# Optimization experiments

Measured on AMD Instinct MI355X. Metric: run time of the kernel, lower is better.

The kernel has to match this reference:

```python
import jax, jax.numpy as jnp
import numpy as np
from jax import lax

SYM = 128
STATES = 2
T = 4194304


def setup_inputs() -> dict:
    key = jax.random.key(0)
    k_tok, k_ls, k_fin = jax.random.split(key, 3)
    tokens = jax.random.randint(k_tok, (T,), 0, SYM, dtype=jnp.int64 if jax.config.jax_enable_x64 else jnp.int32)
    # original init: ones / states / states; add noise so grads are non-degenerate
    ls = jnp.ones((SYM, STATES, STATES), dtype=jnp.float32) / (STATES * STATES)
    ls = ls + 0.01 * jax.random.normal(k_ls, (SYM, STATES, STATES), dtype=jnp.float32)
    final = jnp.ones((STATES, 1), dtype=jnp.float32)
    return {"tokens": tokens, "ls": ls, "final": final}


def reference(tokens, ls, final):
    # initial state vector [1, 0] (hardcoded in the original forward)
    states = ls.shape[1]
    v0 = jnp.zeros((states,), dtype=ls.dtype).at[0].set(1.0)

    def step(v, j):
        # gather the 2x2 transition for symbol j and advance: v <- v @ ls[j]
        return v @ ls[j], None

    v, _ = lax.scan(step, v0, tokens)
    # faithful to the original: the last token's matrix is applied a second time
    v = v @ ls[tokens[-1]]
    return v
```

## Files before the change

kernel.cpp:

```cpp
#include <hip/hip_runtime.h>


#define T_TOKENS 4194304
#define TPB      512
#define TOKS     16
#define BLOCKS   (T_TOKENS / (TPB * TOKS))

typedef float v2f __attribute__((ext_vector_type(2)));

__device__ __forceinline__ float4 mm(const float4 A, const float4 B) {
    const v2f Br0 = {B.x, B.y};
    const v2f Br1 = {B.z, B.w};
    const v2f c0 = A.x * Br0 + A.y * Br1;
    const v2f c1 = A.z * Br0 + A.w * Br1;
    return make_float4(c0.x, c0.y, c1.x, c1.y);
}

template <int N>
__device__ __forceinline__ float4 dpp_shr4(const float4 m) {
    float4 o;
    o.x = __int_as_float(__builtin_amdgcn_update_dpp(
        __float_as_int(m.x), __float_as_int(m.x), 0x110 | N, 0xF, 0xF, false));
    o.y = __int_as_float(__builtin_amdgcn_update_dpp(
        __float_as_int(m.y), __float_as_int(m.y), 0x110 | N, 0xF, 0xF, false));
    o.z = __int_as_float(__builtin_amdgcn_update_dpp(
        __float_as_int(m.z), __float_as_int(m.z), 0x110 | N, 0xF, 0xF, false));
    o.w = __int_as_float(__builtin_amdgcn_update_dpp(
        __float_as_int(m.w), __float_as_int(m.w), 0x110 | N, 0xF, 0xF, false));
    return o;
}

template <int XMASK>
__device__ __forceinline__ float4 swz_xor4(const float4 m) {
    constexpr int OFF = (XMASK << 10) | 0x1F;
    float4 o;
    o.x = __int_as_float(__builtin_amdgcn_ds_swizzle(__float_as_int(m.x), OFF));
    o.y = __int_as_float(__builtin_amdgcn_ds_swizzle(__float_as_int(m.y), OFF));
    o.z = __int_as_float(__builtin_amdgcn_ds_swizzle(__float_as_int(m.z), OFF));
    o.w = __int_as_float(__builtin_amdgcn_ds_swizzle(__float_as_int(m.w), OFF));
    return o;
}

__device__ __forceinline__ float4 wave_reduce_mm(float4 m) {
    m = mm(m, dpp_shr4<1>(m));
    m = mm(m, dpp_shr4<2>(m));
    m = mm(m, dpp_shr4<4>(m));
    m = mm(m, dpp_shr4<8>(m));
    m = mm(m, swz_xor4<16>(m));
    m = mm(m, swz_xor4<32>(m));
    return m;
}

__global__ __launch_bounds__(TPB) void scan_phase1(const int4* __restrict__ tok4,
                                                   const float4* __restrict__ ls,
                                                   float4* __restrict__ partials) {
    __shared__ float4 s_ls[128];
    __shared__ float4 sm[8];

    const int tid = threadIdx.x;
    if (tid < 128) s_ls[tid] = ls[tid];
    __syncthreads();

    const int4* p = tok4 + (size_t)(blockIdx.x * TPB + tid) * (TOKS / 4);
    const int4 t0 = p[0];
    const int4 t1 = p[1];
    const int4 t2 = p[2];
    const int4 t3 = p[3];

    float4 m = s_ls[t0.x];
    m = mm(m, s_ls[t0.y]);
    m = mm(m, s_ls[t0.z]);
    m = mm(m, s_ls[t0.w]);
    m = mm(m, s_ls[t1.x]);
    m = mm(m, s_ls[t1.y]);
    m = mm(m, s_ls[t1.z]);
    m = mm(m, s_ls[t1.w]);
    m = mm(m, s_ls[t2.x]);
    m = mm(m, s_ls[t2.y]);
    m = mm(m, s_ls[t2.z]);
    m = mm(m, s_ls[t2.w]);
    m = mm(m, s_ls[t3.x]);
    m = mm(m, s_ls[t3.y]);
    m = mm(m, s_ls[t3.z]);
    m = mm(m, s_ls[t3.w]);

    m = wave_reduce_mm(m);

    if ((tid & 63) == 0) sm[tid >> 6] = m;
    __syncthreads();
    if (tid == 0) {
        const float4 q01 = mm(sm[0], sm[1]);
        const float4 q23 = mm(sm[2], sm[3]);
        const float4 q45 = mm(sm[4], sm[5]);
        const float4 q67 = mm(sm[6], sm[7]);
        partials[blockIdx.x] = mm(mm(q01, q23), mm(q45, q67));
    }
}

__global__ __launch_bounds__(TPB) void scan_phase2(const float4* __restrict__ partials,
                                                   const int* __restrict__ tokens,
                                                   const float4* __restrict__ ls,
                                                   float* __restrict__ out) {
    const int tid = threadIdx.x;
    float4 m = partials[tid];

    m = wave_reduce_mm(m);

    __shared__ float4 sf[8];
    if ((tid & 63) == 0) sf[tid >> 6] = m;
    __syncthreads();
    if (tid == 0) {
        const float4 q01 = mm(sf[0], sf[1]);
        const float4 q23 = mm(sf[2], sf[3]);
        const float4 q45 = mm(sf[4], sf[5]);
        const float4 q67 = mm(sf[6], sf[7]);
        float4 M = mm(mm(q01, q23), mm(q45, q67));
        M = mm(M, ls[tokens[T_TOKENS - 1]]);
        out[0] = M.x;
        out[1] = M.y;
    }
}

extern "C" void kernel_launch(void* const* d_in, const int* in_sizes, int n_in,
                              void* d_out, int out_size, void* d_ws, size_t ws_size,
                              hipStream_t stream) {
    const int*    tokens = (const int*)d_in[0];
    const float4* ls     = (const float4*)d_in[1];
    float*  out      = (float*)d_out;
    float4* partials = (float4*)d_ws;

    scan_phase1<<<BLOCKS, TPB, 0, stream>>>((const int4*)tokens, ls, partials);
    scan_phase2<<<1, TPB, 0, stream>>>(partials, tokens, ls, out);
}
```

Before: 66.95 us.

## Double tokens per thread, split LDS rows, and use row_bcast DPP wave reduction

Each thread now multiplies 32 tokens as two independent 16-token chains, which halves the block count and adds instruction-level parallelism. The LDS table is split into two row arrays of float2, and the wave reduction drops ds_swizzle in favour of DPP row_bcast15/31 with the result read from lane 63. Phase 2 shrinks to 256 threads to match the 256 partials. The approach relies on the operand order in the row_bcast reduction being correct for non-commutative matrix products, and longer per-thread work may reduce latency hiding.

```diff
diff --git a/kernel.cpp b/kernel.cpp
--- a/kernel.cpp
+++ b/kernel.cpp
@@ -3,121 +3,126 @@
 
 #define T_TOKENS 4194304
 #define TPB      512
-#define TOKS     16
+#define TOKS     32
 #define BLOCKS   (T_TOKENS / (TPB * TOKS))
+#define TPB2     256
 
 typedef float v2f __attribute__((ext_vector_type(2)));
 
-__device__ __forceinline__ float4 mm(const float4 A, const float4 B) {
-    const v2f Br0 = {B.x, B.y};
-    const v2f Br1 = {B.z, B.w};
-    const v2f c0 = A.x * Br0 + A.y * Br1;
-    const v2f c1 = A.z * Br0 + A.w * Br1;
-    return make_float4(c0.x, c0.y, c1.x, c1.y);
+struct m22 { v2f r0, r1; };
+
+__device__ __forceinline__ m22 mm(const m22 A, const m22 B) {
+    m22 C;
+    C.r0 = A.r0.x * B.r0 + A.r0.y * B.r1;
+    C.r1 = A.r1.x * B.r0 + A.r1.y * B.r1;
+    return C;
 }
 
-template <int N>
-__device__ __forceinline__ float4 dpp_shr4(const float4 m) {
-    float4 o;
-    o.x = __int_as_float(__builtin_amdgcn_update_dpp(
-        __float_as_int(m.x), __float_as_int(m.x), 0x110 | N, 0xF, 0xF, false));
-    o.y = __int_as_float(__builtin_amdgcn_update_dpp(
-        __float_as_int(m.y), __float_as_int(m.y), 0x110 | N, 0xF, 0xF, false));
-    o.z = __int_as_float(__builtin_amdgcn_update_dpp(
-        __float_as_int(m.z), __float_as_int(m.z), 0x110 | N, 0xF, 0xF, false));
-    o.w = __int_as_float(__builtin_amdgcn_update_dpp(
-        __float_as_int(m.w), __float_as_int(m.w), 0x110 | N, 0xF, 0xF, false));
+__device__ __forceinline__ float4 to4(const m22 m) {
+    return make_float4(m.r0.x, m.r0.y, m.r1.x, m.r1.y);
+}
+__device__ __forceinline__ m22 fr4(const float4 f) {
+    return m22{ (v2f){f.x, f.y}, (v2f){f.z, f.w} };
+}
+
+template <int CTRL, int ROWM>
+__device__ __forceinline__ m22 dpp4(const m22 m) {
+    m22 o;
+    o.r0.x = __int_as_float(__builtin_amdgcn_update_dpp(
+        __float_as_int(m.r0.x), __float_as_int(m.r0.x), CTRL, ROWM, 0xF, false));
+    o.r0.y = __int_as_float(__builtin_amdgcn_update_dpp(
+        __float_as_int(m.r0.y), __float_as_int(m.r0.y), CTRL, ROWM, 0xF, false));
+    o.r1.x = __int_as_float(__builtin_amdgcn_update_dpp(
+        __float_as_int(m.r1.x), __float_as_int(m.r1.x), CTRL, ROWM, 0xF, false));
+    o.r1.y = __int_as_float(__builtin_amdgcn_update_dpp(
+        __float_as_int(m.r1.y), __float_as_int(m.r1.y), CTRL, ROWM, 0xF, false));
     return o;
 }
 
-template <int XMASK>
-__device__ __forceinline__ float4 swz_xor4(const float4 m) {
-    constexpr int OFF = (XMASK << 10) | 0x1F;
-    float4 o;
-    o.x = __int_as_float(__builtin_amdgcn_ds_swizzle(__float_as_int(m.x), OFF));
-    o.y = __int_as_float(__builtin_amdgcn_ds_swizzle(__float_as_int(m.y), OFF));
-    o.z = __int_as_float(__builtin_amdgcn_ds_swizzle(__float_as_int(m.z), OFF));
-    o.w = __int_as_float(__builtin_amdgcn_ds_swizzle(__float_as_int(m.w), OFF));
-    return o;
-}
-
-__device__ __forceinline__ float4 wave_reduce_mm(float4 m) {
-    m = mm(m, dpp_shr4<1>(m));
-    m = mm(m, dpp_shr4<2>(m));
-    m = mm(m, dpp_shr4<4>(m));
-    m = mm(m, dpp_shr4<8>(m));
-    m = mm(m, swz_xor4<16>(m));
-    m = mm(m, swz_xor4<32>(m));
+__device__ __forceinline__ m22 wave_reduce_hi(m22 m) {
+    m = mm(dpp4<0x101, 0xF>(m), m);
+    m = mm(dpp4<0x102, 0xF>(m), m);
+    m = mm(dpp4<0x104, 0xF>(m), m);
+    m = mm(dpp4<0x108, 0xF>(m), m);
+    m = mm(dpp4<0x142, 0xA>(m), m);
+    m = mm(dpp4<0x143, 0xC>(m), m);
     return m;
 }
 
 __global__ __launch_bounds__(TPB) void scan_phase1(const int4* __restrict__ tok4,
                                                    const float4* __restrict__ ls,
                                                    float4* __restrict__ partials) {
-    __shared__ float4 s_ls[128];
+    __shared__ v2f s_r0[128];
+    __shared__ v2f s_r1[128];
     __shared__ float4 sm[8];
 
     const int tid = threadIdx.x;
-    if (tid < 128) s_ls[tid] = ls[tid];
+    if (tid < 128) {
+        const float4 e = ls[tid];
+        s_r0[tid] = (v2f){e.x, e.y};
+        s_r1[tid] = (v2f){e.z, e.w};
+    }
     __syncthreads();
+
+#define LDM(i) (m22{ s_r0[(i)], s_r1[(i)] })
 
     const int4* p = tok4 + (size_t)(blockIdx.x * TPB + tid) * (TOKS / 4);
     const int4 t0 = p[0];
     const int4 t1 = p[1];
     const int4 t2 = p[2];
     const int4 t3 = p[3];
+    const int4 t4 = p[4];
+    const int4 t5 = p[5];
+    const int4 t6 = p[6];
+    const int4 t7 = p[7];
 
-    float4 m = s_ls[t0.x];
-    m = mm(m, s_ls[t0.y]);
-    m = mm(m, s_ls[t0.z]);
-    m = mm(m, s_ls[t0.w]);
-    m = mm(m, s_ls[t1.x]);
-    m = mm(m, s_ls[t1.y]);
-    m = mm(m, s_ls[t1.z]);
-    m = mm(m, s_ls[t1.w]);
-    m = mm(m, s_ls[t2.x]);
-    m = mm(m, s_ls[t2.y]);
-    m = mm(m, s_ls[t2.z]);
-    m = mm(m, s_ls[t2.w]);
-    m = mm(m, s_ls[t3.x]);
-    m = mm(m, s_ls[t3.y]);
-    m = mm(m, s_ls[t3.z]);
-    m = mm(m, s_ls[t3.w]);
+    m22 a = LDM(t0.x);
+    a = mm(a, LDM(t0.y)); a = mm(a, LDM(t0.z)); a = mm(a, LDM(t0.w));
+    a = mm(a, LDM(t1.x)); a = mm(a, LDM(t1.y)); a = mm(a, LDM(t1.z)); a = mm(a, LDM(t1.w));
+    a = mm(a, LDM(t2.x)); a = mm(a, LDM(t2.y)); a = mm(a, LDM(t2.z)); a = mm(a, LDM(t2.w));
+    a = mm(a, LDM(t3.x)); a = mm(a, LDM(t3.y)); a = mm(a, LDM(t3.z)); a = mm(a, LDM(t3.w));
 
-    m = wave_reduce_mm(m);
+    m22 b = LDM(t4.x);
+    b = mm(b, LDM(t4.y)); b = mm(b, LDM(t4.z)); b = mm(b, LDM(t4.w));
+    b = mm(b, LDM(t5.x)); b = mm(b, LDM(t5.y)); b = mm(b, LDM(t5.z)); b = mm(b, LDM(t5.w));
+    b = mm(b, LDM(t6.x)); b = mm(b, LDM(t6.y)); b = mm(b, LDM(t6.z)); b = mm(b, LDM(t6.w));
+    b = mm(b, LDM(t7.x)); b = mm(b, LDM(t7.y)); b = mm(b, LDM(t7.z)); b = mm(b, LDM(t7.w));
 
-    if ((tid & 63) == 0) sm[tid >> 6] = m;
+    m22 m = mm(a, b);
+
+    m = wave_reduce_hi(m);
+
+    if ((tid & 63) == 63) sm[tid >> 6] = to4(m);
     __syncthreads();
     if (tid == 0) {
-        const float4 q01 = mm(sm[0], sm[1]);
-        const float4 q23 = mm(sm[2], sm[3]);
-        const float4 q45 = mm(sm[4], sm[5]);
-        const float4 q67 = mm(sm[6], sm[7]);
-        partials[blockIdx.x] = mm(mm(q01, q23), mm(q45, q67));
+        const m22 q01 = mm(fr4(sm[0]), fr4(sm[1]));
+        const m22 q23 = mm(fr4(sm[2]), fr4(sm[3]));
+        const m22 q45 = mm(fr4(sm[4]), fr4(sm[5]));
+        const m22 q67 = mm(fr4(sm[6]), fr4(sm[7]));
+        partials[blockIdx.x] = to4(mm(mm(q01, q23), mm(q45, q67)));
     }
+#undef LDM
 }
 
-__global__ __launch_bounds__(TPB) void scan_phase2(const float4* __restrict__ partials,
-                                                   const int* __restrict__ tokens,
-                                                   const float4* __restrict__ ls,
-                                                   float* __restrict__ out) {
+__global__ __launch_bounds__(TPB2) void scan_phase2(const float4* __restrict__ partials,
+                                                    const int* __restrict__ tokens,
+                                                    const float4* __restrict__ ls,
+                                                    float* __restrict__ out) {
     const int tid = threadIdx.x;
-    float4 m = partials[tid];
+    m22 m = fr4(partials[tid]);
 
-    m = wave_reduce_mm(m);
+    m = wave_reduce_hi(m);
 
-    __shared__ float4 sf[8];
-    if ((tid & 63) == 0) sf[tid >> 6] = m;
+    __shared__ float4 sf[4];
+    if ((tid & 63) == 63) sf[tid >> 6] = to4(m);
     __syncthreads();
     if (tid == 0) {
-        const float4 q01 = mm(sf[0], sf[1]);
-        const float4 q23 = mm(sf[2], sf[3]);
-        const float4 q45 = mm(sf[4], sf[5]);
-        const float4 q67 = mm(sf[6], sf[7]);
-        float4 M = mm(mm(q01, q23), mm(q45, q67));
-        M = mm(M, ls[tokens[T_TOKENS - 1]]);
-        out[0] = M.x;
-        out[1] = M.y;
+        const m22 q01 = mm(fr4(sf[0]), fr4(sf[1]));
+        const m22 q23 = mm(fr4(sf[2]), fr4(sf[3]));
+        m22 M = mm(q01, q23);
+        M = mm(M, fr4(ls[tokens[T_TOKENS - 1]]));
+        out[0] = M.r0.x;
+        out[1] = M.r0.y;
     }
 }
 
@@ -130,5 +135,5 @@
     float4* partials = (float4*)d_ws;
 
     scan_phase1<<<BLOCKS, TPB, 0, stream>>>((const int4*)tokens, ls, partials);
-    scan_phase2<<<1, TPB, 0, stream>>>(partials, tokens, ls, out);
+    scan_phase2<<<1, TPB2, 0, stream>>>(partials, tokens, ls, out);
 }
```

New measurement: 69.89 us. 1.04x slower.
